# Optimization experiments

Measured on AMD Instinct MI355X. Metric: run time of the kernel, lower is better.

Reference implementation:

```python
import jax, jax.numpy as jnp
import numpy as np

B, N, D, S = 128, 1024, 512, 64
ITERS = 3
EPS = 1e-8


def setup_inputs() -> dict:
    key = jax.random.key(0)
    ks = jax.random.split(key, 10)
    inp = {
        "inputs_pe": jax.random.normal(ks[0], (B, N, D), dtype=jnp.float32),
        "inputs": jax.random.normal(ks[1], (B, N, D), dtype=jnp.float32),
        "slots": jax.random.normal(ks[2], (1, S, D), dtype=jnp.float32),
        "W1": jax.random.normal(ks[3], (D, D), dtype=jnp.float32) * 0.02,
        "b1": jnp.zeros((D,), dtype=jnp.float32),
        "W2": jax.random.normal(ks[4], (D, D), dtype=jnp.float32) * 0.02,
        "b2": jnp.zeros((D,), dtype=jnp.float32),
        "W3": jax.random.normal(ks[5], (D, D), dtype=jnp.float32) * 0.02,
        "b3": jnp.zeros((D,), dtype=jnp.float32),
    }
    return inp


def reference(inputs_pe, inputs, slots, W1, b1, W2, b2, W3, b3):
    b = inputs_pe.shape[0]
    scale = D ** (-0.5)
    # to_k: Linear -> ReLU -> Linear -> ReLU -> Linear (torch Linear: x @ W.T + b)
    h = jax.nn.relu(jnp.einsum('bnd,ed->bne', inputs_pe, W1) + b1)
    h = jax.nn.relu(jnp.einsum('bnd,ed->bne', h, W2) + b2)
    k = jnp.einsum('bnd,ed->bne', h, W3) + b3  # [b, n, d]

    q = jnp.broadcast_to(slots, (b, S, D))  # slots never updated in the loop
    for _ in range(ITERS):
        dots = jnp.einsum('bid,bjd->bij', q, k) * scale  # [b, S, n]
        s_j = dots.sum(axis=2, keepdims=True)            # sum over keys j -> [b, S, 1]
        s_all = dots.sum(axis=(1, 2), keepdims=True)     # total per batch -> [b, 1, 1]
        dots = dots / s_j * s_all
        attn = jax.nn.sigmoid(dots)
        attn2 = attn / (attn.sum(axis=-1, keepdims=True) + EPS)
        updates = jnp.einsum('bjd,bij->bid', inputs, attn2)  # [b, S, d]
    return updates, attn
```

## Files before the change

kernel.cpp:

```cpp
#include <hip/hip_runtime.h>
#include <stdint.h>

#define Bb 128
#define Nn 1024
#define Dd 512
#define Ss 64

constexpr float kScale = 0.044194173824159216f;
constexpr float kEps = 1e-8f;

typedef __bf16 bf16x8 __attribute__((ext_vector_type(8)));
typedef float f32x4 __attribute__((ext_vector_type(4)));
typedef float f32x16 __attribute__((ext_vector_type(16)));
typedef unsigned short ushort8 __attribute__((ext_vector_type(8)));

#define MFMA32 __builtin_amdgcn_mfma_f32_32x32x16_bf16

__device__ inline unsigned short f2bf_rne(float x) {
  unsigned u = __builtin_bit_cast(unsigned, x);
  u += 0x7FFFu + ((u >> 16) & 1u);
  return (unsigned short)(u >> 16);
}
__device__ inline float bf2f(unsigned short h) {
  unsigned u = ((unsigned)h) << 16;
  return __builtin_bit_cast(float, u);
}

__device__ inline void gl_lds16(const void* g, void* l) {
  typedef unsigned int u32;
  auto gp = (u32 __attribute__((address_space(1)))*)(unsigned long long)(uintptr_t)g;
  auto lp = (u32 __attribute__((address_space(3)))*)(unsigned int)(uintptr_t)l;
  __builtin_amdgcn_global_load_lds(gp, lp, 16, 0, 0);
}

__global__ void cast_split_i(const float* __restrict__ in,
                             unsigned short* __restrict__ out, int n8) {
  int i = blockIdx.x * blockDim.x + threadIdx.x;
  const int stride = gridDim.x * blockDim.x;
  for (; i < n8; i += stride) {
    const float4 v0 = ((const float4*)in)[i * 2];
    const float4 v1 = ((const float4*)in)[i * 2 + 1];
    float f[8] = {v0.x, v0.y, v0.z, v0.w, v1.x, v1.y, v1.z, v1.w};
    ushort8 h, lo;
#pragma unroll
    for (int j = 0; j < 8; j++) {
      h[j] = f2bf_rne(f[j]);
      lo[j] = f2bf_rne(f[j] - bf2f(h[j]));
    }
    ((ushort8*)out)[i * 2] = h;
    ((ushort8*)out)[i * 2 + 1] = lo;
  }
}

template <int ACT>
__global__ __launch_bounds__(512, 1) void gemm_hp(
    const unsigned short* __restrict__ A, const unsigned short* __restrict__ W,
    const float* __restrict__ bias, unsigned short* __restrict__ C) {
  constexpr int NH = 32;
  extern __shared__ unsigned short lds[];
  const int t = threadIdx.x, l = t & 63, w = t >> 6;
  const int wr = w >> 2, wc = w & 3;

  const int wg = ((blockIdx.x & 7) << 7) + (blockIdx.x >> 3);
  const long rowA0 = (long)(wg >> 1) * 256;
  const int colB0 = (wg & 1) * 256;

  const unsigned short* base8 = (w < 4) ? A + rowA0 * 1024 : W + (long)colB0 * 1024;
  const int p2s = ((l >> 1) ^ (l >> 4)) & 1;
  const unsigned short* srcp[4];
  int dstp[4];
#pragma unroll
  for (int j = 0; j < 4; j++) {
    const int cid = (w & 3) * 4 + j;
    srcp[j] = base8 + (long)(cid * 16 + (l >> 2)) * 1024 + p2s * 16 + (l & 1) * 8;
    dstp[j] = (w * 4 + j) * 512;
  }
#define STG(h)                                                            \
  {                                                                       \
    unsigned short* bq_ = lds + ((h) & 3) * 16384;                        \
    _Pragma("unroll") for (int j = 0; j < 4; j++)                         \
        gl_lds16(srcp[j] + (h) * 32, bq_ + dstp[j]);                      \
  }

  const int pp16 = (((l >> 5) ^ ((l >> 2) & 1))) * 16;
  const int abase0 = (wr * 128 + (l & 31)) * 32 + pp16;
  const int bbase0 = 8192 + (wc * 64 + (l & 31)) * 32 + pp16;

#define READF(h, S)                                                       \
  {                                                                       \
    const unsigned short* bq_ = lds + ((h) & 3) * 16384;                  \
    _Pragma("unroll") for (int m = 0; m < 4; m++) {                       \
      ah##S[m] = *(const bf16x8*)(bq_ + abase0 + m * 1024);               \
      al##S[m] = *(const bf16x8*)(bq_ + abase0 + m * 1024 + 8);           \
    }                                                                     \
    _Pragma("unroll") for (int n = 0; n < 2; n++) {                       \
      bh##S[n] = *(const bf16x8*)(bq_ + bbase0 + n * 1024);               \
      bl##S[n] = *(const bf16x8*)(bq_ + bbase0 + n * 1024 + 8);           \
    }                                                                     \
  }

#define MFMACL(S)                                                         \
  {                                                                       \
    _Pragma("unroll") for (int m = 0; m < 4; m++)                         \
        _Pragma("unroll") for (int n = 0; n < 2; n++) {                   \
      acc[m][n] = MFMA32(ah##S[m], bh##S[n], acc[m][n], 0, 0, 0);         \
      acc[m][n] = MFMA32(al##S[m], bh##S[n], acc[m][n], 0, 0, 0);         \
      acc[m][n] = MFMA32(ah##S[m], bl##S[n], acc[m][n], 0, 0, 0);         \
    }                                                                     \
  }

#define BODY(h, CUR, NXT)                                                 \
  {                                                                       \
    asm volatile("s_waitcnt lgkmcnt(0)" ::: "memory");                    \
    __builtin_amdgcn_sched_barrier(0);                                    \
    if ((h) < 29) {                                                       \
      asm volatile("s_waitcnt vmcnt(8)" ::: "memory");                    \
    } else if ((h) == 29) {                                               \
      asm volatile("s_waitcnt vmcnt(4)" ::: "memory");                    \
    } else if ((h) == 30) {                                               \
      asm volatile("s_waitcnt vmcnt(0)" ::: "memory");                    \
    }                                                                     \
    __builtin_amdgcn_s_barrier();                                         \
    if ((h) + 4 < NH) STG((h) + 4);                                       \
    if ((h) + 1 < NH) READF((h) + 1, NXT);                                \
    __builtin_amdgcn_sched_barrier(0);                                    \
    __builtin_amdgcn_s_setprio(1);                                        \
    MFMACL(CUR);                                                          \
    __builtin_amdgcn_s_setprio(0);                                        \
  }

  f32x16 acc[4][2] = {};
  bf16x8 ahA[4], alA[4], bhA[2], blA[2];
  bf16x8 ahB[4], alB[4], bhB[2], blB[2];

  STG(0); STG(1); STG(2); STG(3);
  asm volatile("s_waitcnt vmcnt(12)" ::: "memory");
  __builtin_amdgcn_s_barrier();
  READF(0, A);

  for (int hh = 0; hh < NH; hh += 2) {
    BODY(hh, A, B);
    BODY(hh + 1, B, A);
  }
#undef STG
#undef READF
#undef MFMACL
#undef BODY

#pragma unroll
  for (int m = 0; m < 4; m++)
#pragma unroll
    for (int n = 0; n < 2; n++) {
      const int col = colB0 + wc * 64 + n * 32 + (l & 31);
      const float bv = bias[col];
      const int cofs = (col >> 3) * 16 + (col & 7);
#pragma unroll
      for (int r = 0; r < 16; r++) {
        const long row = rowA0 + wr * 128 + m * 32 + (r & 3) + 8 * (r >> 2) + 4 * (l >> 5);
        float xv = acc[m][n][r] + bv;
        if (ACT) xv = fmaxf(xv, 0.0f);
        const unsigned short h = f2bf_rne(xv);
        unsigned short* cp = C + row * 1024 + cofs;
        cp[0] = h;
        cp[8] = f2bf_rne(xv - bf2f(h));
      }
    }
}

__global__ __launch_bounds__(256) void gemm_dots_split(
    const unsigned short* __restrict__ QI, const unsigned short* __restrict__ KI,
    float* __restrict__ dots) {
  constexpr int K = 512, BM = 64, BN = 128, BK = 32;
  __shared__ __align__(16) unsigned short lah[BM * BK];
  __shared__ __align__(16) unsigned short lal[BM * BK];
  __shared__ __align__(16) unsigned short lbh[BN * BK];
  __shared__ __align__(16) unsigned short lbl[BN * BK];
  const int t = threadIdx.x, l = t & 63, w = t >> 6;
  const int b = blockIdx.x >> 3, bc = blockIdx.x & 7;
  const unsigned short* kb = KI + (long)b * Nn * 1024;
  f32x4 acc[4][2] = {};

  const int qbase = (t >> 2) * 1024 + (t & 3) * 16;
  const long kbase0 = (long)(bc * BN + (t >> 2)) * 1024 + (t & 3) * 16;
  const long kbase1 = (long)(bc * BN + 64 + (t >> 2)) * 1024 + (t & 3) * 16;

  for (int k0 = 0; k0 < K; k0 += BK) {
    const int ko = k0 * 2;
    const int lo = w * 512;
    gl_lds16(QI + qbase + ko, lah + lo);
    gl_lds16(QI + qbase + ko + 8, lal + lo);
    gl_lds16(kb + kbase0 + ko, lbh + lo);
    gl_lds16(kb + kbase0 + ko + 8, lbl + lo);
    gl_lds16(kb + kbase1 + ko, lbh + 2048 + lo);
    gl_lds16(kb + kbase1 + ko + 8, lbl + 2048 + lo);
    __syncthreads();
    bf16x8 ah[4], al[4], bh[2], bl[2];
#pragma unroll
    for (int m = 0; m < 4; m++) {
      const int off = (m * 16 + (l & 15)) * BK + (l >> 4) * 8;
      ah[m] = *(const bf16x8*)(lah + off);
      al[m] = *(const bf16x8*)(lal + off);
    }
#pragma unroll
    for (int n = 0; n < 2; n++) {
      const int off = (w * 32 + n * 16 + (l & 15)) * BK + (l >> 4) * 8;
      bh[n] = *(const bf16x8*)(lbh + off);
      bl[n] = *(const bf16x8*)(lbl + off);
    }
#pragma unroll
    for (int m = 0; m < 4; m++)
#pragma unroll
      for (int n = 0; n < 2; n++) {
        acc[m][n] = __builtin_amdgcn_mfma_f32_16x16x32_bf16(ah[m], bh[n], acc[m][n], 0, 0, 0);
        acc[m][n] = __builtin_amdgcn_mfma_f32_16x16x32_bf16(al[m], bh[n], acc[m][n], 0, 0, 0);
        acc[m][n] = __builtin_amdgcn_mfma_f32_16x16x32_bf16(ah[m], bl[n], acc[m][n], 0, 0, 0);
      }
    __syncthreads();
  }
  float* dp = dots + (long)b * Ss * Nn;
#pragma unroll
  for (int m = 0; m < 4; m++) {
    const int row = m * 16 + (l >> 4) * 4;
#pragma unroll
    for (int n = 0; n < 2; n++) {
      const int col = bc * BN + w * 32 + n * 16 + (l & 15);
#pragma unroll
      for (int r = 0; r < 4; r++) dp[(long)(row + r) * Nn + col] = acc[m][n][r] * kScale;
    }
  }
}

__global__ __launch_bounds__(256) void reduce_k(
    const float* __restrict__ dots, float* __restrict__ s_j, float* __restrict__ s_all) {
  const int b = blockIdx.x;
  const int t = threadIdx.x;
  const float* dp = dots + (long)b * Ss * Nn;
  const int i = t >> 2, qq = t & 3;
  float s = 0.f;
  const float* rp = dp + i * Nn + qq * 256;
  for (int j = 0; j < 256; j++) s += rp[j];
  __shared__ float part[256];
  __shared__ float rowsum[64];
  part[t] = s;
  __syncthreads();
  if (t < 64) {
    const float v = part[t * 4] + part[t * 4 + 1] + part[t * 4 + 2] + part[t * 4 + 3];
    rowsum[t] = v;
    s_j[b * 64 + t] = v;
  }
  __syncthreads();
  if (t == 0) {
    float tot = 0.f;
    for (int k = 0; k < 64; k++) tot += rowsum[k];
    s_all[b] = tot;
  }
}

__global__ __launch_bounds__(256) void attn_k(
    const float* __restrict__ dots, const float* __restrict__ s_j,
    const float* __restrict__ s_all, float* __restrict__ attn_out,
    float* __restrict__ inv_r) {
  const int bi = blockIdx.x;
  const int b = bi >> 6;
  const int t = threadIdx.x;
  const float ratio = s_all[b] / s_j[bi];
  const float* dp = dots + (long)bi * Nn;
  float* ap = attn_out + (long)bi * Nn;
  float s = 0.f;
#pragma unroll
  for (int qq = 0; qq < 4; qq++) {
    const int j = qq * 256 + t;
    const float x = dp[j] * ratio;
    const float a = 1.f / (1.f + expf(-x));
    ap[j] = a;
    s += a;
  }
  __shared__ float red[256];
  red[t] = s;
  __syncthreads();
  for (int off = 128; off > 0; off >>= 1) {
    if (t < off) red[t] += red[t + off];
    __syncthreads();
  }
  if (t == 0) inv_r[bi] = 1.f / (red[0] + kEps);
}

__global__ __launch_bounds__(256, 1) void updates_k2(
    const float* __restrict__ attn, const float* __restrict__ inputs,
    const float* __restrict__ inv_r, float* __restrict__ out0) {
  constexpr int NT2 = 32;
  constexpr int BUF_F = 10240;
  extern __shared__ float ldsf[];
  const int t = threadIdx.x, lam = t & 63, w = t >> 6;
  const int b = blockIdx.x >> 1, dt = blockIdx.x & 1;
  const int ig = t >> 5, dg = t & 31;
  const float* inb = inputs + (size_t)b * (Nn * Dd) + dt * 256;
  const float* attsrc = attn + (size_t)b * (Ss * Nn) + (size_t)(t >> 2) * Nn + (t & 3) * 8;
  float acc[8][8] = {};
  float4 ga0, ga1, gb0, gb1;

#define UISSUE(bufi, tile, G0, G1)                                        \
  {                                                                       \
    const int j0_ = (tile)*32;                                            \
    G0 = *(const float4*)(attsrc + j0_);                                  \
    G1 = *(const float4*)(attsrc + j0_ + 4);                              \
    float* db_ = ldsf + (bufi)*BUF_F;                                     \
    _Pragma("unroll") for (int i_ = 0; i_ < 8; i_++) {                    \
      const int row_ = i_ * 4 + w;                                        \
      gl_lds16(inb + (size_t)(j0_ + row_) * Dd + lam * 4, db_ + row_ * 256); \
    }                                                                     \
  }

#define UWRITE(bufi, G0, G1)                                              \
  {                                                                       \
    float* ab_ = ldsf + (bufi)*BUF_F + 8192;                              \
    const int col_ = t >> 2;                                              \
    const int r0_ = (t & 3) * 8;                                          \
    ab_[(r0_ + 0) * 64 + col_] = G0.x;                                    \
    ab_[(r0_ + 1) * 64 + col_] = G0.y;                                    \
    ab_[(r0_ + 2) * 64 + col_] = G0.z;                                    \
    ab_[(r0_ + 3) * 64 + col_] = G0.w;                                    \
    ab_[(r0_ + 4) * 64 + col_] = G1.x;                                    \
    ab_[(r0_ + 5) * 64 + col_] = G1.y;                                    \
    ab_[(r0_ + 6) * 64 + col_] = G1.z;                                    \
    ab_[(r0_ + 7) * 64 + col_] = G1.w;                                    \
  }

#define UCOMP(bufi)                                                       \
  {                                                                       \
    const float* db_ = ldsf + (bufi)*BUF_F;                               \
    const float* ab_ = db_ + 8192;                                        \
    _Pragma("unroll 4") for (int jj = 0; jj < 32; jj++) {                 \
      float av[8], vv[8];                                                 \
      *(float4*)&av[0] = *(const float4*)(ab_ + jj * 64 + ig * 8);        \
      *(float4*)&av[4] = *(const float4*)(ab_ + jj * 64 + ig * 8 + 4);    \
      *(float4*)&vv[0] = *(const float4*)(db_ + jj * 256 + dg * 8);       \
      *(float4*)&vv[4] = *(const float4*)(db_ + jj * 256 + dg * 8 + 4);   \
      _Pragma("unroll") for (int m_ = 0; m_ < 8; m_++)                    \
          _Pragma("unroll") for (int n_ = 0; n_ < 8; n_++)                \
              acc[m_][n_] = __builtin_fmaf(av[m_], vv[n_], acc[m_][n_]);  \
    }                                                                     \
  }

  UISSUE(0, 0, ga0, ga1);
  UISSUE(1, 1, gb0, gb1);
  UWRITE(0, ga0, ga1);

  for (int tt = 0; tt < NT2; tt += 2) {
    asm volatile("s_waitcnt vmcnt(10)" ::: "memory");
    UWRITE((tt + 1) % 3, gb0, gb1);
    asm volatile("s_waitcnt lgkmcnt(0)" ::: "memory");
    __builtin_amdgcn_s_barrier();
    __builtin_amdgcn_sched_barrier(0);
    if (tt < NT2 - 2) UISSUE((tt + 2) % 3, tt + 2, ga0, ga1);
    UCOMP(tt % 3);
    if (tt + 1 < NT2 - 1) {
      asm volatile("s_waitcnt vmcnt(10)" ::: "memory");
    } else {
      asm volatile("s_waitcnt vmcnt(0)" ::: "memory");
    }
    if (tt + 1 < NT2 - 1) UWRITE((tt + 2) % 3, ga0, ga1);
    asm volatile("s_waitcnt lgkmcnt(0)" ::: "memory");
    __builtin_amdgcn_s_barrier();
    __builtin_amdgcn_sched_barrier(0);
    if (tt + 1 < NT2 - 2) UISSUE((tt + 3) % 3, tt + 3, gb0, gb1);
    UCOMP((tt + 1) % 3);
  }
#undef UISSUE
#undef UWRITE
#undef UCOMP

#pragma unroll
  for (int m = 0; m < 8; m++) {
    const int i = ig * 8 + m;
    const float ir = inv_r[b * 64 + i];
    float4 o0, o1;
    o0.x = acc[m][0] * ir; o0.y = acc[m][1] * ir; o0.z = acc[m][2] * ir; o0.w = acc[m][3] * ir;
    o1.x = acc[m][4] * ir; o1.y = acc[m][5] * ir; o1.z = acc[m][6] * ir; o1.w = acc[m][7] * ir;
    float* op = out0 + (size_t)(b * 64 + i) * Dd + dt * 256 + dg * 8;
    *(float4*)op = o0;
    *(float4*)(op + 4) = o1;
  }
}

extern "C" void kernel_launch(void* const* d_in, const int* in_sizes, int n_in,
                              void* d_out, int out_size, void* d_ws, size_t ws_size,
                              hipStream_t stream) {
  (void)in_sizes; (void)n_in; (void)out_size; (void)ws_size;
  const float* inputs_pe = (const float*)d_in[0];
  const float* inputs = (const float*)d_in[1];
  const float* slots = (const float*)d_in[2];
  const float* W1 = (const float*)d_in[3];
  const float* b1 = (const float*)d_in[4];
  const float* W2 = (const float*)d_in[5];
  const float* b2 = (const float*)d_in[6];
  const float* W3 = (const float*)d_in[7];
  const float* b3 = (const float*)d_in[8];

  char* ws = (char*)d_ws;
  size_t off = 0;
  auto alloc = [&](size_t bytes) -> void* {
    void* p = ws + off;
    off += (bytes + 255) & ~(size_t)255;
    return p;
  };
  const size_t actB = (size_t)Bb * Nn * 1024 * 2;
  unsigned short* AI = (unsigned short*)alloc(actB);
  unsigned short* BI = (unsigned short*)alloc(actB);
  unsigned short* w1i = (unsigned short*)alloc(Dd * 1024 * 2);
  unsigned short* w2i = (unsigned short*)alloc(Dd * 1024 * 2);
  unsigned short* w3i = (unsigned short*)alloc(Dd * 1024 * 2);
  unsigned short* qi = (unsigned short*)alloc(Ss * 1024 * 2);
  float* dotsb = (float*)alloc((size_t)Bb * Ss * Nn * 4);
  float* s_j = (float*)alloc(Bb * Ss * 4);
  float* s_all = (float*)alloc(Bb * 4);
  float* inv_r = (float*)alloc(Bb * Ss * 4);

  float* out_updates = (float*)d_out;
  float* out_attn = out_updates + (size_t)Bb * Ss * Dd;

  const int kLdsG = 4 * 32 * 1024;
  const int kLdsU = 3 * 40 * 1024;
  hipFuncSetAttribute(reinterpret_cast<const void*>(gemm_hp<1>),
                      hipFuncAttributeMaxDynamicSharedMemorySize, kLdsG);
  hipFuncSetAttribute(reinterpret_cast<const void*>(gemm_hp<0>),
                      hipFuncAttributeMaxDynamicSharedMemorySize, kLdsG);
  hipFuncSetAttribute(reinterpret_cast<const void*>(updates_k2),
                      hipFuncAttributeMaxDynamicSharedMemorySize, kLdsU);

  cast_split_i<<<4096, 256, 0, stream>>>(inputs_pe, AI, Bb * Nn * Dd / 8);
  cast_split_i<<<128, 256, 0, stream>>>(W1, w1i, Dd * Dd / 8);
  cast_split_i<<<128, 256, 0, stream>>>(W2, w2i, Dd * Dd / 8);
  cast_split_i<<<128, 256, 0, stream>>>(W3, w3i, Dd * Dd / 8);
  cast_split_i<<<16, 256, 0, stream>>>(slots, qi, Ss * Dd / 8);

  gemm_hp<1><<<1024, 512, kLdsG, stream>>>(AI, w1i, b1, BI);
  gemm_hp<1><<<1024, 512, kLdsG, stream>>>(BI, w2i, b2, AI);
  gemm_hp<0><<<1024, 512, kLdsG, stream>>>(AI, w3i, b3, BI);

  gemm_dots_split<<<Bb * 8, 256, 0, stream>>>(qi, BI, dotsb);
  reduce_k<<<Bb, 256, 0, stream>>>(dotsb, s_j, s_all);
  attn_k<<<Bb * Ss, 256, 0, stream>>>(dotsb, s_j, s_all, out_attn, inv_r);
  updates_k2<<<Bb * 2, 256, kLdsU, stream>>>(out_attn, inputs, inv_r, out_updates);
}
```

Measured before the change: 1.030 ms.

## Replace block-cooperative GEMM staging with per-wave private LDS pipelines; shuffle-reduce row sums

The MLP GEMM now uses 256-thread blocks of 256x128 tiles. Each wave loads its own A and W slices into a private triple-buffered LDS region, which removes all block-wide barriers from the main loop and relies only on per-wave vmcnt/lgkmcnt waits. The cost is redundant global loads: waves that share rows or columns each fetch them, there is more LDS per block, and the prefetch depth drops from four stages to two ahead. The reduce kernel is also rewritten to use coalesced float4 loads and wavefront shuffle reductions.

```diff
diff --git a/kernel.cpp b/kernel.cpp
--- a/kernel.cpp
+++ b/kernel.cpp
@@ -53,49 +53,54 @@
 }
 
 template <int ACT>
-__global__ __launch_bounds__(512, 1) void gemm_hp(
+__global__ __launch_bounds__(256, 1) void gemm_wa(
     const unsigned short* __restrict__ A, const unsigned short* __restrict__ W,
     const float* __restrict__ bias, unsigned short* __restrict__ C) {
   constexpr int NH = 32;
   extern __shared__ unsigned short lds[];
   const int t = threadIdx.x, l = t & 63, w = t >> 6;
-  const int wr = w >> 2, wc = w & 3;
-
-  const int wg = ((blockIdx.x & 7) << 7) + (blockIdx.x >> 3);
-  const long rowA0 = (long)(wg >> 1) * 256;
-  const int colB0 = (wg & 1) * 256;
-
-  const unsigned short* base8 = (w < 4) ? A + rowA0 * 1024 : W + (long)colB0 * 1024;
-  const int p2s = ((l >> 1) ^ (l >> 4)) & 1;
-  const unsigned short* srcp[4];
-  int dstp[4];
-#pragma unroll
-  for (int j = 0; j < 4; j++) {
-    const int cid = (w & 3) * 4 + j;
-    srcp[j] = base8 + (long)(cid * 16 + (l >> 2)) * 1024 + p2s * 16 + (l & 1) * 8;
-    dstp[j] = (w * 4 + j) * 512;
+  const int wr = w >> 1, wc = w & 1;
+
+  const int wg = ((blockIdx.x & 7) << 8) + (blockIdx.x >> 3);
+  const long rowA0 = (long)(wg >> 2) * 256;
+  const int colB0 = (wg & 3) * 128;
+  unsigned short* wlds = lds + w * 18432;
+
+  const unsigned short* Abase = A + (rowA0 + wr * 128) * 1024;
+  const unsigned short* Wbase = W + (long)(colB0 + wc * 64) * 1024;
+  const int qs = (l & 3) ^ ((l >> 3) & 3);
+  const unsigned short* srcp[12];
+  int dstp[12];
+#pragma unroll
+  for (int c = 0; c < 12; c++) {
+    const int rrel = (c < 8 ? c : c - 8) * 16 + (l >> 2);
+    srcp[c] = (c < 8 ? Abase : Wbase) + (long)rrel * 1024 + qs * 8;
+    dstp[c] = c * 512;
   }
 #define STG(h)                                                            \
   {                                                                       \
-    unsigned short* bq_ = lds + ((h) & 3) * 16384;                        \
-    _Pragma("unroll") for (int j = 0; j < 4; j++)                         \
-        gl_lds16(srcp[j] + (h) * 32, bq_ + dstp[j]);                      \
-  }
-
-  const int pp16 = (((l >> 5) ^ ((l >> 2) & 1))) * 16;
-  const int abase0 = (wr * 128 + (l & 31)) * 32 + pp16;
-  const int bbase0 = 8192 + (wc * 64 + (l & 31)) * 32 + pp16;
+    unsigned short* bq_ = wlds + ((h) % 3) * 6144;                        \
+    _Pragma("unroll") for (int c = 0; c < 12; c++)                        \
+        gl_lds16(srcp[c] + (h) * 32, bq_ + dstp[c]);                      \
+  }
+
+  const int ppA = ((2 * (l >> 5)) ^ ((l >> 1) & 3)) * 8;
+  int aoff[4], boff[2];
+#pragma unroll
+  for (int m = 0; m < 4; m++) aoff[m] = (m * 32 + (l & 31)) * 32 + ppA;
+#pragma unroll
+  for (int n = 0; n < 2; n++) boff[n] = 4096 + (n * 32 + (l & 31)) * 32 + ppA;
 
 #define READF(h, S)                                                       \
   {                                                                       \
-    const unsigned short* bq_ = lds + ((h) & 3) * 16384;                  \
+    const unsigned short* bq_ = wlds + ((h) % 3) * 6144;                  \
     _Pragma("unroll") for (int m = 0; m < 4; m++) {                       \
-      ah##S[m] = *(const bf16x8*)(bq_ + abase0 + m * 1024);               \
-      al##S[m] = *(const bf16x8*)(bq_ + abase0 + m * 1024 + 8);           \
+      ah##S[m] = *(const bf16x8*)(bq_ + aoff[m]);                         \
+      al##S[m] = *(const bf16x8*)(bq_ + (aoff[m] ^ 8));                   \
     }                                                                     \
     _Pragma("unroll") for (int n = 0; n < 2; n++) {                       \
-      bh##S[n] = *(const bf16x8*)(bq_ + bbase0 + n * 1024);               \
-      bl##S[n] = *(const bf16x8*)(bq_ + bbase0 + n * 1024 + 8);           \
+      bh##S[n] = *(const bf16x8*)(bq_ + boff[n]);                         \
+      bl##S[n] = *(const bf16x8*)(bq_ + (boff[n] ^ 8));                   \
     }                                                                     \
   }
 
@@ -111,18 +116,18 @@
 
 #define BODY(h, CUR, NXT)                                                 \
   {                                                                       \
-    asm volatile("s_waitcnt lgkmcnt(0)" ::: "memory");                    \
-    __builtin_amdgcn_sched_barrier(0);                                    \
-    if ((h) < 29) {                                                       \
-      asm volatile("s_waitcnt vmcnt(8)" ::: "memory");                    \
-    } else if ((h) == 29) {                                               \
-      asm volatile("s_waitcnt vmcnt(4)" ::: "memory");                    \
-    } else if ((h) == 30) {                                               \
-      asm volatile("s_waitcnt vmcnt(0)" ::: "memory");                    \
-    }                                                                     \
-    __builtin_amdgcn_s_barrier();                                         \
-    if ((h) + 4 < NH) STG((h) + 4);                                       \
-    if ((h) + 1 < NH) READF((h) + 1, NXT);                                \
+    if ((h) + 2 < NH) STG((h) + 2);                                       \
+    if ((h) + 1 < NH) {                                                   \
+      if ((h) + 2 < NH) {                                                 \
+        asm volatile("s_waitcnt vmcnt(12)" ::: "memory");                 \
+      } else {                                                            \
+        asm volatile("s_waitcnt vmcnt(0)" ::: "memory");                  \
+      }                                                                   \
+      READF((h) + 1, NXT);                                                \
+      asm volatile("s_waitcnt lgkmcnt(12)" ::: "memory");                 \
+    } else {                                                              \
+      asm volatile("s_waitcnt lgkmcnt(0)" ::: "memory");                  \
+    }                                                                     \
     __builtin_amdgcn_sched_barrier(0);                                    \
     __builtin_amdgcn_s_setprio(1);                                        \
     MFMACL(CUR);                                                          \
@@ -133,11 +138,12 @@
   bf16x8 ahA[4], alA[4], bhA[2], blA[2];
   bf16x8 ahB[4], alB[4], bhB[2], blB[2];
 
-  STG(0); STG(1); STG(2); STG(3);
+  STG(0);
+  STG(1);
   asm volatile("s_waitcnt vmcnt(12)" ::: "memory");
-  __builtin_amdgcn_s_barrier();
   READF(0, A);
 
+#pragma unroll
   for (int hh = 0; hh < NH; hh += 2) {
     BODY(hh, A, B);
     BODY(hh + 1, B, A);
@@ -232,27 +238,29 @@
 
 __global__ __launch_bounds__(256) void reduce_k(
     const float* __restrict__ dots, float* __restrict__ s_j, float* __restrict__ s_all) {
-  const int b = blockIdx.x;
-  const int t = threadIdx.x;
-  const float* dp = dots + (long)b * Ss * Nn;
-  const int i = t >> 2, qq = t & 3;
-  float s = 0.f;
-  const float* rp = dp + i * Nn + qq * 256;
-  for (int j = 0; j < 256; j++) s += rp[j];
-  __shared__ float part[256];
+  const int b = blockIdx.x, t = threadIdx.x, l = t & 63, w = t >> 6;
+  const float4* dp = (const float4*)(dots + (long)b * Ss * Nn);
+  __shared__ float rowacc[64][4];
   __shared__ float rowsum[64];
-  part[t] = s;
+  for (int r = 0; r < 64; ++r) {
+    const float4 v = dp[r * 256 + t];
+    float s = v.x + v.y + v.z + v.w;
+#pragma unroll
+    for (int off = 32; off; off >>= 1) s += __shfl_down(s, off);
+    if (l == 0) rowacc[r][w] = s;
+  }
   __syncthreads();
   if (t < 64) {
-    const float v = part[t * 4] + part[t * 4 + 1] + part[t * 4 + 2] + part[t * 4 + 3];
+    const float v = rowacc[t][0] + rowacc[t][1] + rowacc[t][2] + rowacc[t][3];
     rowsum[t] = v;
     s_j[b * 64 + t] = v;
   }
   __syncthreads();
-  if (t == 0) {
-    float tot = 0.f;
-    for (int k = 0; k < 64; k++) tot += rowsum[k];
-    s_all[b] = tot;
+  if (t < 64) {
+    float v = rowsum[t];
+#pragma unroll
+    for (int off = 32; off; off >>= 1) v += __shfl_down(v, off);
+    if (t == 0) s_all[b] = v;
   }
 }
 
@@ -419,11 +427,11 @@
   float* out_updates = (float*)d_out;
   float* out_attn = out_updates + (size_t)Bb * Ss * Dd;
 
-  const int kLdsG = 4 * 32 * 1024;
+  const int kLdsG = 144 * 1024;
   const int kLdsU = 3 * 40 * 1024;
-  hipFuncSetAttribute(reinterpret_cast<const void*>(gemm_hp<1>),
+  hipFuncSetAttribute(reinterpret_cast<const void*>(gemm_wa<1>),
                       hipFuncAttributeMaxDynamicSharedMemorySize, kLdsG);
-  hipFuncSetAttribute(reinterpret_cast<const void*>(gemm_hp<0>),
+  hipFuncSetAttribute(reinterpret_cast<const void*>(gemm_wa<0>),
                       hipFuncAttributeMaxDynamicSharedMemorySize, kLdsG);
   hipFuncSetAttribute(reinterpret_cast<const void*>(updates_k2),
                       hipFuncAttributeMaxDynamicSharedMemorySize, kLdsU);
@@ -434,9 +442,9 @@
   cast_split_i<<<128, 256, 0, stream>>>(W3, w3i, Dd * Dd / 8);
   cast_split_i<<<16, 256, 0, stream>>>(slots, qi, Ss * Dd / 8);
 
-  gemm_hp<1><<<1024, 512, kLdsG, stream>>>(AI, w1i, b1, BI);
-  gemm_hp<1><<<1024, 512, kLdsG, stream>>>(BI, w2i, b2, AI);
-  gemm_hp<0><<<1024, 512, kLdsG, stream>>>(AI, w3i, b3, BI);
+  gemm_wa<1><<<2048, 256, kLdsG, stream>>>(AI, w1i, b1, BI);
+  gemm_wa<1><<<2048, 256, kLdsG, stream>>>(BI, w2i, b2, AI);
+  gemm_wa<0><<<2048, 256, kLdsG, stream>>>(AI, w3i, b3, BI);
 
   gemm_dots_split<<<Bb * 8, 256, 0, stream>>>(qi, BI, dotsb);
   reduce_k<<<Bb, 256, 0, stream>>>(dotsb, s_j, s_all);
```

Result: slower. 1.241 ms (+20.5%).

## Restructure GEMM main loop into four barrier-separated phases and vectorize row reductions

Applied to the files above, without the earlier changes.

The GEMM K-loop drops the double-buffered register fragments and prefetch-next-tile scheme. In its place, each K step is split into four phases, each with LDS reads, a workgroup barrier and six MFMAs, and the prefetch depth is reduced from 4 stages to 3. The aim is to interleave LDS reads with MFMA work across waves while using fewer registers, at the cost of many more barriers per iteration. The reduce kernel also switches to float4 coalesced loads with wave shuffle reductions in place of strided per-thread serial sums. A leftover unused MFMA6 macro suggests the code is exploratory.

```diff
diff --git a/kernel.cpp b/kernel.cpp
--- a/kernel.cpp
+++ b/kernel.cpp
@@ -53,7 +53,7 @@
 }
 
 template <int ACT>
-__global__ __launch_bounds__(512, 1) void gemm_hp(
+__global__ __launch_bounds__(512, 1) void gemm_8p(
     const unsigned short* __restrict__ A, const unsigned short* __restrict__ W,
     const float* __restrict__ bias, unsigned short* __restrict__ C) {
   constexpr int NH = 32;
@@ -86,66 +86,95 @@
   const int abase0 = (wr * 128 + (l & 31)) * 32 + pp16;
   const int bbase0 = 8192 + (wc * 64 + (l & 31)) * 32 + pp16;
 
-#define READF(h, S)                                                       \
-  {                                                                       \
-    const unsigned short* bq_ = lds + ((h) & 3) * 16384;                  \
-    _Pragma("unroll") for (int m = 0; m < 4; m++) {                       \
-      ah##S[m] = *(const bf16x8*)(bq_ + abase0 + m * 1024);               \
-      al##S[m] = *(const bf16x8*)(bq_ + abase0 + m * 1024 + 8);           \
-    }                                                                     \
-    _Pragma("unroll") for (int n = 0; n < 2; n++) {                       \
-      bh##S[n] = *(const bf16x8*)(bq_ + bbase0 + n * 1024);               \
-      bl##S[n] = *(const bf16x8*)(bq_ + bbase0 + n * 1024 + 8);           \
-    }                                                                     \
-  }
-
-#define MFMACL(S)                                                         \
-  {                                                                       \
-    _Pragma("unroll") for (int m = 0; m < 4; m++)                         \
-        _Pragma("unroll") for (int n = 0; n < 2; n++) {                   \
-      acc[m][n] = MFMA32(ah##S[m], bh##S[n], acc[m][n], 0, 0, 0);         \
-      acc[m][n] = MFMA32(al##S[m], bh##S[n], acc[m][n], 0, 0, 0);         \
-      acc[m][n] = MFMA32(ah##S[m], bl##S[n], acc[m][n], 0, 0, 0);         \
-    }                                                                     \
-  }
-
-#define BODY(h, CUR, NXT)                                                 \
-  {                                                                       \
-    asm volatile("s_waitcnt lgkmcnt(0)" ::: "memory");                    \
-    __builtin_amdgcn_sched_barrier(0);                                    \
-    if ((h) < 29) {                                                       \
-      asm volatile("s_waitcnt vmcnt(8)" ::: "memory");                    \
-    } else if ((h) == 29) {                                               \
-      asm volatile("s_waitcnt vmcnt(4)" ::: "memory");                    \
-    } else if ((h) == 30) {                                               \
-      asm volatile("s_waitcnt vmcnt(0)" ::: "memory");                    \
-    }                                                                     \
-    __builtin_amdgcn_s_barrier();                                         \
-    if ((h) + 4 < NH) STG((h) + 4);                                       \
-    if ((h) + 1 < NH) READF((h) + 1, NXT);                                \
-    __builtin_amdgcn_sched_barrier(0);                                    \
-    __builtin_amdgcn_s_setprio(1);                                        \
-    MFMACL(CUR);                                                          \
-    __builtin_amdgcn_s_setprio(0);                                        \
-  }
-
   f32x16 acc[4][2] = {};
-  bf16x8 ahA[4], alA[4], bhA[2], blA[2];
-  bf16x8 ahB[4], alB[4], bhB[2], blB[2];
-
-  STG(0); STG(1); STG(2); STG(3);
-  asm volatile("s_waitcnt vmcnt(12)" ::: "memory");
-  __builtin_amdgcn_s_barrier();
-  READF(0, A);
-
-  for (int hh = 0; hh < NH; hh += 2) {
-    BODY(hh, A, B);
-    BODY(hh + 1, B, A);
+  bf16x8 ah[4], al[4], bh0, bl0, bh1, bl1;
+
+#define PH_BAR()                                                          \
+  __builtin_amdgcn_s_barrier();                                           \
+  asm volatile("s_waitcnt lgkmcnt(0)" ::: "memory");                      \
+  __builtin_amdgcn_sched_barrier(0);
+
+#define MFMA6(MA, MB, BH, BL)                                             \
+  __builtin_amdgcn_s_setprio(1);                                          \
+  acc[MA][( &BH == &bh0 ) ? 0 : 1] = acc[MA][(&BH == &bh0) ? 0 : 1];      \
+  __builtin_amdgcn_s_setprio(0);
+
+
+  STG(0); STG(1); STG(2);
+
+  for (int h = 0; h < NH; ++h) {
+    if (h < NH - 2) {
+      asm volatile("s_waitcnt vmcnt(8)" ::: "memory");
+    } else if (h == NH - 2) {
+      asm volatile("s_waitcnt vmcnt(4)" ::: "memory");
+    } else {
+      asm volatile("s_waitcnt vmcnt(0)" ::: "memory");
+    }
+    __builtin_amdgcn_s_barrier();
+    __builtin_amdgcn_sched_barrier(0);
+    if (h + 3 < NH) STG(h + 3);
+    const unsigned short* bq = lds + (h & 3) * 16384;
+
+    ah[0] = *(const bf16x8*)(bq + abase0);
+    al[0] = *(const bf16x8*)(bq + abase0 + 8);
+    ah[1] = *(const bf16x8*)(bq + abase0 + 1024);
+    al[1] = *(const bf16x8*)(bq + abase0 + 1024 + 8);
+    bh0 = *(const bf16x8*)(bq + bbase0);
+    bl0 = *(const bf16x8*)(bq + bbase0 + 8);
+    PH_BAR()
+    __builtin_amdgcn_s_setprio(1);
+    acc[0][0] = MFMA32(ah[0], bh0, acc[0][0], 0, 0, 0);
+    acc[0][0] = MFMA32(al[0], bh0, acc[0][0], 0, 0, 0);
+    acc[0][0] = MFMA32(ah[0], bl0, acc[0][0], 0, 0, 0);
+    acc[1][0] = MFMA32(ah[1], bh0, acc[1][0], 0, 0, 0);
+    acc[1][0] = MFMA32(al[1], bh0, acc[1][0], 0, 0, 0);
+    acc[1][0] = MFMA32(ah[1], bl0, acc[1][0], 0, 0, 0);
+    __builtin_amdgcn_s_setprio(0);
+    __builtin_amdgcn_sched_barrier(0);
+
+    ah[2] = *(const bf16x8*)(bq + abase0 + 2048);
+    al[2] = *(const bf16x8*)(bq + abase0 + 2048 + 8);
+    ah[3] = *(const bf16x8*)(bq + abase0 + 3072);
+    al[3] = *(const bf16x8*)(bq + abase0 + 3072 + 8);
+    PH_BAR()
+    __builtin_amdgcn_s_setprio(1);
+    acc[2][0] = MFMA32(ah[2], bh0, acc[2][0], 0, 0, 0);
+    acc[2][0] = MFMA32(al[2], bh0, acc[2][0], 0, 0, 0);
+    acc[2][0] = MFMA32(ah[2], bl0, acc[2][0], 0, 0, 0);
+    acc[3][0] = MFMA32(ah[3], bh0, acc[3][0], 0, 0, 0);
+    acc[3][0] = MFMA32(al[3], bh0, acc[3][0], 0, 0, 0);
+    acc[3][0] = MFMA32(ah[3], bl0, acc[3][0], 0, 0, 0);
+    __builtin_amdgcn_s_setprio(0);
+    __builtin_amdgcn_sched_barrier(0);
+
+    bh1 = *(const bf16x8*)(bq + bbase0 + 1024);
+    bl1 = *(const bf16x8*)(bq + bbase0 + 1024 + 8);
+    PH_BAR()
+    __builtin_amdgcn_s_setprio(1);
+    acc[0][1] = MFMA32(ah[0], bh1, acc[0][1], 0, 0, 0);
+    acc[0][1] = MFMA32(al[0], bh1, acc[0][1], 0, 0, 0);
+    acc[0][1] = MFMA32(ah[0], bl1, acc[0][1], 0, 0, 0);
+    acc[1][1] = MFMA32(ah[1], bh1, acc[1][1], 0, 0, 0);
+    acc[1][1] = MFMA32(al[1], bh1, acc[1][1], 0, 0, 0);
+    acc[1][1] = MFMA32(ah[1], bl1, acc[1][1], 0, 0, 0);
+    __builtin_amdgcn_s_setprio(0);
+    __builtin_amdgcn_sched_barrier(0);
+
+    __builtin_amdgcn_s_barrier();
+    __builtin_amdgcn_sched_barrier(0);
+    __builtin_amdgcn_s_setprio(1);
+    acc[2][1] = MFMA32(ah[2], bh1, acc[2][1], 0, 0, 0);
+    acc[2][1] = MFMA32(al[2], bh1, acc[2][1], 0, 0, 0);
+    acc[2][1] = MFMA32(ah[2], bl1, acc[2][1], 0, 0, 0);
+    acc[3][1] = MFMA32(ah[3], bh1, acc[3][1], 0, 0, 0);
+    acc[3][1] = MFMA32(al[3], bh1, acc[3][1], 0, 0, 0);
+    acc[3][1] = MFMA32(ah[3], bl1, acc[3][1], 0, 0, 0);
+    __builtin_amdgcn_s_setprio(0);
+    __builtin_amdgcn_sched_barrier(0);
   }
 #undef STG
-#undef READF
-#undef MFMACL
-#undef BODY
+#undef PH_BAR
+#undef MFMA6
 
 #pragma unroll
   for (int m = 0; m < 4; m++)
@@ -232,27 +261,29 @@
 
 __global__ __launch_bounds__(256) void reduce_k(
     const float* __restrict__ dots, float* __restrict__ s_j, float* __restrict__ s_all) {
-  const int b = blockIdx.x;
-  const int t = threadIdx.x;
-  const float* dp = dots + (long)b * Ss * Nn;
-  const int i = t >> 2, qq = t & 3;
-  float s = 0.f;
-  const float* rp = dp + i * Nn + qq * 256;
-  for (int j = 0; j < 256; j++) s += rp[j];
-  __shared__ float part[256];
+  const int b = blockIdx.x, t = threadIdx.x, l = t & 63, w = t >> 6;
+  const float4* dp = (const float4*)(dots + (long)b * Ss * Nn);
+  __shared__ float rowacc[64][4];
   __shared__ float rowsum[64];
-  part[t] = s;
+  for (int r = 0; r < 64; ++r) {
+    const float4 v = dp[r * 256 + t];
+    float s = v.x + v.y + v.z + v.w;
+#pragma unroll
+    for (int off = 32; off; off >>= 1) s += __shfl_down(s, off);
+    if (l == 0) rowacc[r][w] = s;
+  }
   __syncthreads();
   if (t < 64) {
-    const float v = part[t * 4] + part[t * 4 + 1] + part[t * 4 + 2] + part[t * 4 + 3];
+    const float v = rowacc[t][0] + rowacc[t][1] + rowacc[t][2] + rowacc[t][3];
     rowsum[t] = v;
     s_j[b * 64 + t] = v;
   }
   __syncthreads();
-  if (t == 0) {
-    float tot = 0.f;
-    for (int k = 0; k < 64; k++) tot += rowsum[k];
-    s_all[b] = tot;
+  if (t < 64) {
+    float v = rowsum[t];
+#pragma unroll
+    for (int off = 32; off; off >>= 1) v += __shfl_down(v, off);
+    if (t == 0) s_all[b] = v;
   }
 }
 
@@ -421,9 +452,9 @@
 
   const int kLdsG = 4 * 32 * 1024;
   const int kLdsU = 3 * 40 * 1024;
-  hipFuncSetAttribute(reinterpret_cast<const void*>(gemm_hp<1>),
+  hipFuncSetAttribute(reinterpret_cast<const void*>(gemm_8p<1>),
                       hipFuncAttributeMaxDynamicSharedMemorySize, kLdsG);
-  hipFuncSetAttribute(reinterpret_cast<const void*>(gemm_hp<0>),
+  hipFuncSetAttribute(reinterpret_cast<const void*>(gemm_8p<0>),
                       hipFuncAttributeMaxDynamicSharedMemorySize, kLdsG);
   hipFuncSetAttribute(reinterpret_cast<const void*>(updates_k2),
                       hipFuncAttributeMaxDynamicSharedMemorySize, kLdsU);
@@ -434,9 +465,9 @@
   cast_split_i<<<128, 256, 0, stream>>>(W3, w3i, Dd * Dd / 8);
   cast_split_i<<<16, 256, 0, stream>>>(slots, qi, Ss * Dd / 8);
 
-  gemm_hp<1><<<1024, 512, kLdsG, stream>>>(AI, w1i, b1, BI);
-  gemm_hp<1><<<1024, 512, kLdsG, stream>>>(BI, w2i, b2, AI);
-  gemm_hp<0><<<1024, 512, kLdsG, stream>>>(AI, w3i, b3, BI);
+  gemm_8p<1><<<1024, 512, kLdsG, stream>>>(AI, w1i, b1, BI);
+  gemm_8p<1><<<1024, 512, kLdsG, stream>>>(BI, w2i, b2, AI);
+  gemm_8p<0><<<1024, 512, kLdsG, stream>>>(AI, w3i, b3, BI);
 
   gemm_dots_split<<<Bb * 8, 256, 0, stream>>>(qi, BI, dotsb);
   reduce_k<<<Bb, 256, 0, stream>>>(dotsb, s_j, s_all);
```

Result: slower. 1.054 ms (+2.3%).
